# Optimization experiments

Hardware: AMD Instinct MI355X
Metric: run time of the kernel (lower is better)

Reference implementation:

```python
import jax, jax.numpy as jnp
import numpy as np

N, E = 100000, 800000
HID, H, D = 128, 4, 32  # hidden, heads, head_dim (HID = H*D)
NODE_IN, EDGE_IN, NL = 12, 3, 4
EPS_LN = 1e-5


def _ln(x, g, b):
    mu = jnp.mean(x, axis=-1, keepdims=True)
    var = jnp.var(x, axis=-1, keepdims=True)
    return (x - mu) * jax.lax.rsqrt(var + EPS_LN) * g + b


def _gatv2(h, src, dst, e, Wl, bl, Wr, br, We, att, bias):
    # GATv2Conv (PyG semantics): lin_l -> source (x_j), lin_r -> target (x_i)
    xl = (h @ Wl + bl).reshape(-1, H, D)          # (N,H,D) source proj
    xr = (h @ Wr + br).reshape(-1, H, D)          # (N,H,D) target proj
    ee = (e @ We).reshape(-1, H, D)               # (E,H,D) edge proj (no bias in PyG)
    m = xl[src] + xr[dst] + ee                    # (E,H,D)
    score = jnp.einsum('ehd,hd->eh', jax.nn.leaky_relu(m, 0.2), att)  # (E,H)
    smax = jax.ops.segment_max(score, dst, num_segments=N)            # (N,H)
    ex = jnp.exp(score - smax[dst])
    den = jax.ops.segment_sum(ex, dst, num_segments=N)
    alpha = ex / (den[dst] + 1e-16)               # per-destination softmax
    msg = xl[src] * alpha[..., None]              # (E,H,D)
    out = jax.ops.segment_sum(msg, dst, num_segments=N).reshape(-1, H * D)
    return out + bias


def _forward(x, edge_attr, edge_proj_w, edge_proj_b,
             l0_Wl, l0_bl, l0_Wr, l0_br, l0_We, l0_att, l0_bias,
             Wl, bl, Wr, br, We, att, bias, ln_g, ln_b, edge_index):
    src, dst = edge_index[0], edge_index[1]
    e = jax.nn.silu(edge_attr @ edge_proj_w + edge_proj_b)  # (E,HID)
    # layer 0 (12 -> 128): no residual since shapes differ
    hn = _gatv2(x, src, dst, e, l0_Wl, l0_bl, l0_Wr, l0_br, l0_We, l0_att, l0_bias)
    h = jax.nn.silu(_ln(hn, ln_g[0], ln_b[0]))
    for i in range(NL - 1):  # layers 1..3 with residual
        hn = _gatv2(h, src, dst, e, Wl[i], bl[i], Wr[i], br[i], We[i], att[i], bias[i])
        h = h + jax.nn.silu(_ln(hn, ln_g[i + 1], ln_b[i + 1]))
    return h


def setup_inputs():
    key = jax.random.key(0)
    ks = jax.random.split(key, 32)
    g = lambda i, shape, s: (jax.random.normal(ks[i], shape, jnp.float32) * s)
    inp = {
        'x': jax.random.uniform(ks[0], (N, NODE_IN), jnp.float32),
        'edge_index': jax.random.randint(ks[1], (2, E), 0, N, jnp.int32),
        'edge_attr': jax.random.normal(ks[2], (E, EDGE_IN), jnp.float32),
        'edge_proj_w': g(3, (EDGE_IN, HID), 0.3),
        'edge_proj_b': jnp.zeros((HID,), jnp.float32),
        'l0_Wl': g(4, (NODE_IN, HID), 0.2),
        'l0_bl': jnp.zeros((HID,), jnp.float32),
        'l0_Wr': g(5, (NODE_IN, HID), 0.2),
        'l0_br': jnp.zeros((HID,), jnp.float32),
        'l0_We': g(6, (HID, HID), 0.08),
        'l0_att': g(7, (H, D), 0.15),
        'l0_bias': jnp.zeros((HID,), jnp.float32),
        'Wl': g(8, (NL - 1, HID, HID), 0.08),
        'bl': jnp.zeros((NL - 1, HID), jnp.float32),
        'Wr': g(9, (NL - 1, HID, HID), 0.08),
        'br': jnp.zeros((NL - 1, HID), jnp.float32),
        'We': g(10, (NL - 1, HID, HID), 0.08),
        'att': g(11, (NL - 1, H, D), 0.15),
        'bias': jnp.zeros((NL - 1, HID), jnp.float32),
        'ln_g': jnp.ones((NL, HID), jnp.float32),
        'ln_b': jnp.zeros((NL, HID), jnp.float32),
    }
    return inp


def reference(x, edge_index, edge_attr, edge_proj_w, edge_proj_b,
              l0_Wl, l0_bl, l0_Wr, l0_br, l0_We, l0_att, l0_bias,
              Wl, bl, Wr, br, We, att, bias, ln_g, ln_b):
    return _forward(x, edge_attr, edge_proj_w, edge_proj_b,
                    l0_Wl, l0_bl, l0_Wr, l0_br, l0_We, l0_att, l0_bias,
                    Wl, bl, Wr, br, We, att, bias, ln_g, ln_b, edge_index)
```

## Files before the change

### kernel.cpp

```cpp
#include <hip/hip_runtime.h>
#include <hip/hip_bf16.h>


using bf16x8 = __attribute__((ext_vector_type(8))) short;
using f32x4  = __attribute__((ext_vector_type(4))) float;

__device__ inline unsigned short f2bf(float x) {
  __hip_bfloat16 h = __float2bfloat16(x);
  return *reinterpret_cast<unsigned short*>(&h);
}
__device__ inline float bf2f(unsigned short u) {
  unsigned int x = ((unsigned int)u) << 16;
  return __uint_as_float(x);
}

__global__ __launch_bounds__(256) void count_kernel(const int* __restrict__ dstv,
                                                    int* __restrict__ deg, int E) {
  int e = blockIdx.x * 256 + threadIdx.x;
  if (e < E) atomicAdd(&deg[dstv[e]], 1);
}

__global__ __launch_bounds__(1024) void scan_local_kernel(
    const int* __restrict__ deg, int* __restrict__ off,
    int* __restrict__ bsum, int n) {
  __shared__ int wsum[16];
  int t = threadIdx.x;
  int lane = t & 63, wid = t >> 6;
  int i = blockIdx.x * 1024 + t;
  int v = (i < n) ? deg[i] : 0;
  int x = v;
  #pragma unroll
  for (int o = 1; o < 64; o <<= 1) {
    int y = __shfl_up(x, o, 64);
    if (lane >= o) x += y;
  }
  if (lane == 63) wsum[wid] = x;
  __syncthreads();
  if (wid == 0) {
    int w = (lane < 16) ? wsum[lane] : 0;
    #pragma unroll
    for (int o = 1; o < 16; o <<= 1) {
      int y = __shfl_up(w, o, 64);
      if (lane >= o) w += y;
    }
    if (lane < 16) wsum[lane] = w;
  }
  __syncthreads();
  int wbase = (wid == 0) ? 0 : wsum[wid - 1];
  if (i < n) off[i] = wbase + (x - v);
  if (t == 0) bsum[blockIdx.x] = wsum[15];
}

__global__ __launch_bounds__(1024) void scan_bsums_kernel(
    const int* __restrict__ bsum, int* __restrict__ bpre,
    int nb, int* __restrict__ off, int n) {
  __shared__ int wsum[16];
  int t = threadIdx.x;
  int lane = t & 63, wid = t >> 6;
  int v = (t < nb) ? bsum[t] : 0;
  int x = v;
  #pragma unroll
  for (int o = 1; o < 64; o <<= 1) {
    int y = __shfl_up(x, o, 64);
    if (lane >= o) x += y;
  }
  if (lane == 63) wsum[wid] = x;
  __syncthreads();
  if (wid == 0) {
    int w = (lane < 16) ? wsum[lane] : 0;
    #pragma unroll
    for (int o = 1; o < 16; o <<= 1) {
      int y = __shfl_up(w, o, 64);
      if (lane >= o) w += y;
    }
    if (lane < 16) wsum[lane] = w;
  }
  __syncthreads();
  int wbase = (wid == 0) ? 0 : wsum[wid - 1];
  if (t < nb) bpre[t] = wbase + (x - v);
  if (t == 0) off[n] = wsum[15];
}

__global__ __launch_bounds__(256) void scan_addback_kernel(
    int* __restrict__ off, const int* __restrict__ bpre,
    int* __restrict__ cursor, int n) {
  int i = blockIdx.x * 256 + threadIdx.x;
  if (i < n) {
    int v = off[i] + bpre[i >> 10];
    off[i] = v;
    cursor[i] = v;
  }
}

__global__ __launch_bounds__(256) void place_kernel(const int* __restrict__ srcv,
                                                    const int* __restrict__ dstv,
                                                    const float* __restrict__ eattr,
                                                    int* __restrict__ cursor,
                                                    int* __restrict__ ssrc,
                                                    int* __restrict__ sdst,
                                                    float* __restrict__ seattr, int E) {
  int e = blockIdx.x * 256 + threadIdx.x;
  if (e < E) {
    int d = dstv[e];
    int p = atomicAdd(&cursor[d], 1);
    ssrc[p] = srcv[e];
    sdst[p] = d;
    seattr[p * 3 + 0] = eattr[e * 3 + 0];
    seattr[p * 3 + 1] = eattr[e * 3 + 1];
    seattr[p * 3 + 2] = eattr[e * 3 + 2];
  }
}

__global__ __launch_bounds__(256) void wt_kernel(
    const float* __restrict__ l0_We, const float* __restrict__ We,
    const float* __restrict__ Wl, const float* __restrict__ Wr,
    unsigned short* __restrict__ WeT, unsigned short* __restrict__ WlT,
    unsigned short* __restrict__ WrT) {
  int b = blockIdx.x, t = threadIdx.x;
  const float* src;
  unsigned short* dst;
  if (b == 0)      { src = l0_We;              dst = WeT; }
  else if (b < 4)  { src = We + (b - 1) * 16384; dst = WeT + b * 16384; }
  else if (b < 7)  { src = Wl + (b - 4) * 16384; dst = WlT + (b - 4) * 16384; }
  else             { src = Wr + (b - 7) * 16384; dst = WrT + (b - 7) * 16384; }
  int n = t >> 1, k0 = (t & 1) * 64;
  #pragma unroll
  for (int k = 0; k < 64; ++k)
    dst[n * 128 + k0 + k] = f2bf(src[(k0 + k) * 128 + n]);
}

__global__ __launch_bounds__(256) void node_proj0_kernel(
    const float* __restrict__ x,
    const float* __restrict__ Wl, const float* __restrict__ bl,
    const float* __restrict__ Wr, const float* __restrict__ br,
    unsigned short* __restrict__ xl, unsigned short* __restrict__ xr, int N) {
  int idx = blockIdx.x * 256 + threadIdx.x;
  int node = idx >> 7, col = idx & 127;
  if (node >= N) return;
  float al = bl[col], ar = br[col];
  const float* xrow = x + node * 12;
  #pragma unroll
  for (int k = 0; k < 12; ++k) {
    float xv = xrow[k];
    al += xv * Wl[k * 128 + col];
    ar += xv * Wr[k * 128 + col];
  }
  xl[idx] = f2bf(al);
  xr[idx] = f2bf(ar);
}

__global__ __launch_bounds__(256) void node_proj_kernel(
    const unsigned short* __restrict__ hbf,
    const unsigned short* __restrict__ WlT, const float* __restrict__ bl,
    const unsigned short* __restrict__ WrT, const float* __restrict__ br,
    unsigned short* __restrict__ xl, unsigned short* __restrict__ xr, int N) {
  __shared__ unsigned short A_sh[64 * 136];
  int t = threadIdx.x;
  int nb = blockIdx.x * 64;
  #pragma unroll
  for (int it = 0; it < 4; ++it) {
    int idx = it * 256 + t;
    int row = idx >> 4, chunk = idx & 15;
    int ng = nb + row;
    float4 v = make_float4(0.f, 0.f, 0.f, 0.f);
    if (ng < N) v = *(const float4*)(hbf + ng * 128 + chunk * 8);
    *(float4*)(A_sh + row * 136 + chunk * 8) = v;
  }
  __syncthreads();
  int lane = t & 63, w = t >> 6;
  int m = lane & 15, quad = lane >> 4;
  bf16x8 afr[4];
  #pragma unroll
  for (int s = 0; s < 4; ++s)
    afr[s] = *(const bf16x8*)(A_sh + (w * 16 + m) * 136 + s * 32 + quad * 8);
  #pragma unroll
  for (int part = 0; part < 2; ++part) {
    const unsigned short* Bt = part ? WrT : WlT;
    const float* bias = part ? br : bl;
    unsigned short* out = part ? xr : xl;
    f32x4 acc[8];
    #pragma unroll
    for (int tt = 0; tt < 8; ++tt)
      #pragma unroll
      for (int r = 0; r < 4; ++r) acc[tt][r] = 0.f;
    #pragma unroll
    for (int tt = 0; tt < 8; ++tt)
      #pragma unroll
      for (int s = 0; s < 4; ++s) {
        bf16x8 b = *(const bf16x8*)(Bt + (tt * 16 + m) * 128 + s * 32 + quad * 8);
        acc[tt] = __builtin_amdgcn_mfma_f32_16x16x32_bf16(afr[s], b, acc[tt], 0, 0, 0);
      }
    #pragma unroll
    for (int tt = 0; tt < 8; ++tt) {
      int col = tt * 16 + m;
      float bv = bias[col];
      #pragma unroll
      for (int r = 0; r < 4; ++r) {
        int ng = nb + w * 16 + quad * 4 + r;
        if (ng < N) out[ng * 128 + col] = f2bf(acc[tt][r] + bv);
      }
    }
  }
}

__global__ __launch_bounds__(256) void edge_score_kernel(
    const float* __restrict__ seattr,
    const float* __restrict__ Pw,
    const float* __restrict__ Pb,
    const unsigned short* __restrict__ WeT,
    const float* __restrict__ attw,
    const unsigned short* __restrict__ xl, const unsigned short* __restrict__ xr,
    const int* __restrict__ ssrc, const int* __restrict__ sdst,
    float* __restrict__ scores, int E) {
  __shared__ unsigned short ee_sh[64 * 128];
  __shared__ float att_sh[4 * 40];
  __shared__ float pw_sh[512];
  int t = threadIdx.x;
  int eb = blockIdx.x * 64;
  int lane = t & 63, w = t >> 6;
  int m = lane & 15, quad = lane >> 4;

  if (t < 128) att_sh[(t >> 5) * 40 + (t & 31)] = attw[t];
  for (int i = t; i < 512; i += 256) pw_sh[i] = (i < 384) ? Pw[i] : Pb[i - 384];

  int le2 = t >> 2, hh = t & 3;
  int eg = eb + le2;
  int sv = 0, dv = 0;
  if (eg < E) { sv = ssrc[eg]; dv = sdst[eg]; }
  bf16x8 xa[4], xb[4];
  #pragma unroll
  for (int j = 0; j < 4; ++j) {
    xa[j] = *(const bf16x8*)(xl + (size_t)sv * 128 + hh * 32 + j * 8);
    xb[j] = *(const bf16x8*)(xr + (size_t)dv * 128 + hh * 32 + j * 8);
  }
  __builtin_amdgcn_sched_barrier(0);
  __syncthreads();

  int e = eb + w * 16 + m;
  float ea0 = 0.f, ea1 = 0.f, ea2 = 0.f;
  if (e < E) { ea0 = seattr[e * 3]; ea1 = seattr[e * 3 + 1]; ea2 = seattr[e * 3 + 2]; }
  bf16x8 afr[4];
  #pragma unroll
  for (int s = 0; s < 4; ++s) {
    int k0 = s * 32 + quad * 8;
    f32x4 r0a = *(const f32x4*)(pw_sh + k0),       r0b = *(const f32x4*)(pw_sh + k0 + 4);
    f32x4 r1a = *(const f32x4*)(pw_sh + 128 + k0), r1b = *(const f32x4*)(pw_sh + 128 + k0 + 4);
    f32x4 r2a = *(const f32x4*)(pw_sh + 256 + k0), r2b = *(const f32x4*)(pw_sh + 256 + k0 + 4);
    f32x4 r3a = *(const f32x4*)(pw_sh + 384 + k0), r3b = *(const f32x4*)(pw_sh + 384 + k0 + 4);
    union { bf16x8 v; unsigned short u[8]; } af;
    #pragma unroll
    for (int j = 0; j < 4; ++j) {
      float z = ea0 * r0a[j] + ea1 * r1a[j] + ea2 * r2a[j] + r3a[j];
      af.u[j] = f2bf(z * __builtin_amdgcn_rcpf(1.f + __expf(-z)));
      float z2 = ea0 * r0b[j] + ea1 * r1b[j] + ea2 * r2b[j] + r3b[j];
      af.u[j + 4] = f2bf(z2 * __builtin_amdgcn_rcpf(1.f + __expf(-z2)));
    }
    afr[s] = af.v;
  }

  f32x4 acc[8];
  #pragma unroll
  for (int tt = 0; tt < 8; ++tt)
    #pragma unroll
    for (int r = 0; r < 4; ++r) acc[tt][r] = 0.f;
  #pragma unroll
  for (int tt = 0; tt < 8; ++tt)
    #pragma unroll
    for (int s = 0; s < 4; ++s) {
      bf16x8 b = *(const bf16x8*)(WeT + (tt * 16 + m) * 128 + s * 32 + quad * 8);
      acc[tt] = __builtin_amdgcn_mfma_f32_16x16x32_bf16(afr[s], b, acc[tt], 0, 0, 0);
    }

  #pragma unroll
  for (int tt = 0; tt < 8; ++tt) {
    int col = tt * 16 + m;
    int chunk = col >> 3, within = col & 7;
    #pragma unroll
    for (int r = 0; r < 4; ++r) {
      int le = w * 16 + quad * 4 + r;
      int p = chunk ^ (le & 7);
      ee_sh[le * 128 + p * 8 + within] = f2bf(acc[tt][r]);
    }
  }
  __syncthreads();

  if (eg < E) {
    float sc = 0.f;
    #pragma unroll
    for (int cl = 0; cl < 4; ++cl) {
      int p = (hh * 4 + cl) ^ (le2 & 7);
      bf16x8 ev = *(const bf16x8*)(ee_sh + le2 * 128 + p * 8);
      f32x4 av0 = *(const f32x4*)(att_sh + hh * 40 + cl * 8);
      f32x4 av1 = *(const f32x4*)(att_sh + hh * 40 + cl * 8 + 4);
      #pragma unroll
      for (int q = 0; q < 8; ++q) {
        float mv = bf2f((unsigned short)ev[q])
                 + bf2f((unsigned short)xa[cl][q])
                 + bf2f((unsigned short)xb[cl][q]);
        mv = (mv > 0.f) ? mv : 0.2f * mv;
        float aw = (q < 4) ? av0[q] : av1[q - 4];
        sc += mv * aw;
      }
    }
    scores[eg * 4 + hh] = __expf(sc);
  }
}

__global__ __launch_bounds__(256) void aggregate_kernel(
    const unsigned short* __restrict__ xl, const float* __restrict__ scores,
    const int* __restrict__ off, const int* __restrict__ ssrc,
    const float* __restrict__ bias,
    const float* __restrict__ lng, const float* __restrict__ lnb,
    const float* __restrict__ h_in, float* __restrict__ h_out,
    unsigned short* __restrict__ hbf_out, int N) {
  int t = threadIdx.x;
  int wid = t >> 6, lane = t & 63;
  int half = lane >> 5, l32 = lane & 31;
  int n = blockIdx.x * 8 + wid * 2 + half;
  if (n >= N) return;
  int hh = l32 >> 3;
  int col0 = l32 * 4;
  int p0 = off[n], p1 = off[n + 1];
  float den0 = 0.f, den1 = 0.f, den2 = 0.f, den3 = 0.f;
  float a00 = 0.f, a01 = 0.f, a02 = 0.f, a03 = 0.f;
  float a10 = 0.f, a11 = 0.f, a12 = 0.f, a13 = 0.f;
  float a20 = 0.f, a21 = 0.f, a22 = 0.f, a23 = 0.f;
  float a30 = 0.f, a31 = 0.f, a32 = 0.f, a33 = 0.f;
  int p = p0;
  for (; p + 3 < p1; p += 4) {
    float w0 = scores[p * 4 + hh];
    float w1 = scores[(p + 1) * 4 + hh];
    float w2 = scores[(p + 2) * 4 + hh];
    float w3 = scores[(p + 3) * 4 + hh];
    int s0 = ssrc[p], s1 = ssrc[p + 1], s2 = ssrc[p + 2], s3 = ssrc[p + 3];
    ushort4 x0 = *(const ushort4*)(xl + (size_t)s0 * 128 + col0);
    ushort4 x1 = *(const ushort4*)(xl + (size_t)s1 * 128 + col0);
    ushort4 x2 = *(const ushort4*)(xl + (size_t)s2 * 128 + col0);
    ushort4 x3 = *(const ushort4*)(xl + (size_t)s3 * 128 + col0);
    den0 += w0; den1 += w1; den2 += w2; den3 += w3;
    a00 += w0 * bf2f(x0.x); a01 += w0 * bf2f(x0.y); a02 += w0 * bf2f(x0.z); a03 += w0 * bf2f(x0.w);
    a10 += w1 * bf2f(x1.x); a11 += w1 * bf2f(x1.y); a12 += w1 * bf2f(x1.z); a13 += w1 * bf2f(x1.w);
    a20 += w2 * bf2f(x2.x); a21 += w2 * bf2f(x2.y); a22 += w2 * bf2f(x2.z); a23 += w2 * bf2f(x2.w);
    a30 += w3 * bf2f(x3.x); a31 += w3 * bf2f(x3.y); a32 += w3 * bf2f(x3.z); a33 += w3 * bf2f(x3.w);
  }
  for (; p < p1; ++p) {
    float w0 = scores[p * 4 + hh];
    int s0 = ssrc[p];
    ushort4 x0 = *(const ushort4*)(xl + (size_t)s0 * 128 + col0);
    den0 += w0;
    a00 += w0 * bf2f(x0.x); a01 += w0 * bf2f(x0.y); a02 += w0 * bf2f(x0.z); a03 += w0 * bf2f(x0.w);
  }
  float rden = (den0 + den1) + (den2 + den3);
  float c0 = (a00 + a10) + (a20 + a30);
  float c1 = (a01 + a11) + (a21 + a31);
  float c2 = (a02 + a12) + (a22 + a32);
  float c3 = (a03 + a13) + (a23 + a33);
  float inv = 1.f / (rden + 1e-16f);
  const float4 bb = *(const float4*)(bias + col0);
  float v0 = c0 * inv + bb.x;
  float v1 = c1 * inv + bb.y;
  float v2 = c2 * inv + bb.z;
  float v3 = c3 * inv + bb.w;
  float s1 = (v0 + v1) + (v2 + v3);
  float s2 = (v0 * v0 + v1 * v1) + (v2 * v2 + v3 * v3);
  #pragma unroll
  for (int o = 1; o < 32; o <<= 1) {
    s1 += __shfl_xor(s1, o, 64);
    s2 += __shfl_xor(s2, o, 64);
  }
  float mean = s1 * (1.f / 128.f);
  float var = s2 * (1.f / 128.f) - mean * mean;
  float rs = rsqrtf(var + 1e-5f);
  const float4 g4 = *(const float4*)(lng + col0);
  const float4 b4 = *(const float4*)(lnb + col0);
  float y0 = (v0 - mean) * rs * g4.x + b4.x;
  float y1 = (v1 - mean) * rs * g4.y + b4.y;
  float y2 = (v2 - mean) * rs * g4.z + b4.z;
  float y3 = (v3 - mean) * rs * g4.w + b4.w;
  float o0 = y0 / (1.f + __expf(-y0));
  float o1 = y1 / (1.f + __expf(-y1));
  float o2 = y2 / (1.f + __expf(-y2));
  float o3 = y3 / (1.f + __expf(-y3));
  if (h_in) {
    const float4 hv = *(const float4*)(h_in + (size_t)n * 128 + col0);
    o0 += hv.x; o1 += hv.y; o2 += hv.z; o3 += hv.w;
  }
  float4 ov; ov.x = o0; ov.y = o1; ov.z = o2; ov.w = o3;
  *(float4*)(h_out + (size_t)n * 128 + col0) = ov;
  if (hbf_out) {
    ushort4 hb;
    hb.x = f2bf(o0); hb.y = f2bf(o1); hb.z = f2bf(o2); hb.w = f2bf(o3);
    *(ushort4*)(hbf_out + (size_t)n * 128 + col0) = hb;
  }
}

extern "C" void kernel_launch(void* const* d_in, const int* in_sizes, int n_in,
                              void* d_out, int out_size, void* d_ws, size_t ws_size,
                              hipStream_t stream) {
  const float* x       = (const float*)d_in[0];
  const int*   eidx    = (const int*)d_in[1];
  const float* eattr   = (const float*)d_in[2];
  const float* Pw      = (const float*)d_in[3];
  const float* Pb      = (const float*)d_in[4];
  const float* l0_Wl   = (const float*)d_in[5];
  const float* l0_bl   = (const float*)d_in[6];
  const float* l0_Wr   = (const float*)d_in[7];
  const float* l0_br   = (const float*)d_in[8];
  const float* l0_We   = (const float*)d_in[9];
  const float* l0_att  = (const float*)d_in[10];
  const float* l0_bias = (const float*)d_in[11];
  const float* Wl      = (const float*)d_in[12];
  const float* bl      = (const float*)d_in[13];
  const float* Wr      = (const float*)d_in[14];
  const float* br      = (const float*)d_in[15];
  const float* We      = (const float*)d_in[16];
  const float* att     = (const float*)d_in[17];
  const float* bias    = (const float*)d_in[18];
  const float* ln_g    = (const float*)d_in[19];
  const float* ln_b    = (const float*)d_in[20];
  (void)n_in; (void)out_size; (void)ws_size;

  int N = in_sizes[0] / 12;
  int E = in_sizes[2] / 3;
  const int* srcv = eidx;
  const int* dstv = eidx + E;

  char* w = (char*)d_ws;
  unsigned short* xl_bf = (unsigned short*)w; w += (size_t)N * 128 * 2;
  unsigned short* xr_bf = (unsigned short*)w; w += (size_t)N * 128 * 2;
  unsigned short* h_bf  = (unsigned short*)w; w += (size_t)N * 128 * 2;
  float* h      = (float*)w;  w += (size_t)N * 128 * 4;
  float* scores = (float*)w;  w += (size_t)E * 4 * 4;
  float* seattr = (float*)w;  w += (size_t)E * 3 * 4;
  int* ssrc   = (int*)w;      w += (size_t)E * 4;
  int* sdst   = (int*)w;      w += (size_t)E * 4;
  int* deg    = (int*)w;      w += (size_t)N * 4;
  int* off    = (int*)w;      w += (size_t)(N + 1) * 4;
  int* cursor = (int*)w;      w += (size_t)N * 4 + 12;
  unsigned short* WeT = (unsigned short*)w; w += (size_t)4 * 16384 * 2;
  unsigned short* WlT = (unsigned short*)w; w += (size_t)3 * 16384 * 2;
  unsigned short* WrT = (unsigned short*)w; w += (size_t)3 * 16384 * 2;

  int* bsum = (int*)scores;
  int* bpre = (int*)scores + 1024;

  hipMemsetAsync(deg, 0, (size_t)N * 4, stream);
  int gE = (E + 255) / 256;
  count_kernel<<<gE, 256, 0, stream>>>(dstv, deg, E);
  int nb = (N + 1023) / 1024;
  scan_local_kernel<<<nb, 1024, 0, stream>>>(deg, off, bsum, N);
  scan_bsums_kernel<<<1, 1024, 0, stream>>>(bsum, bpre, nb, off, N);
  scan_addback_kernel<<<(N + 255) / 256, 256, 0, stream>>>(off, bpre, cursor, N);
  place_kernel<<<gE, 256, 0, stream>>>(srcv, dstv, eattr, cursor, ssrc, sdst, seattr, E);
  wt_kernel<<<10, 256, 0, stream>>>(l0_We, We, Wl, Wr, WeT, WlT, WrT);

  dim3 egrid((E + 63) / 64);
  dim3 ngrid((N + 63) / 64);
  int agrid = (N + 7) / 8;

  node_proj0_kernel<<<(N * 128 + 255) / 256, 256, 0, stream>>>(
      x, l0_Wl, l0_bl, l0_Wr, l0_br, xl_bf, xr_bf, N);
  edge_score_kernel<<<egrid, 256, 0, stream>>>(
      seattr, Pw, Pb, WeT, l0_att, xl_bf, xr_bf, ssrc, sdst, scores, E);
  aggregate_kernel<<<agrid, 256, 0, stream>>>(
      xl_bf, scores, off, ssrc, l0_bias, ln_g, ln_b, nullptr, h, h_bf, N);

  for (int i = 0; i < 3; ++i) {
    node_proj_kernel<<<ngrid, 256, 0, stream>>>(
        h_bf, WlT + i * 16384, bl + i * 128, WrT + i * 16384, br + i * 128,
        xl_bf, xr_bf, N);
    edge_score_kernel<<<egrid, 256, 0, stream>>>(
        seattr, Pw, Pb, WeT + (i + 1) * 16384, att + i * 128,
        xl_bf, xr_bf, ssrc, sdst, scores, E);
    float* hout = (i == 2) ? (float*)d_out : h;
    unsigned short* hbfout = (i == 2) ? nullptr : h_bf;
    aggregate_kernel<<<agrid, 256, 0, stream>>>(
        xl_bf, scores, off, ssrc, bias + i * 128,
        ln_g + (i + 1) * 128, ln_b + (i + 1) * 128, h, hout, hbfout, N);
  }
}
```

Measured before the change: 1.515 ms.

## Process two edge tiles per block in edge_score, prefetching second tile's gathers

The edge score kernel now handles 128 edges per block in two 64-edge halves. The xl/xr gathers and edge attributes for the second half are issued before scoring the first half, so their latency overlaps with compute. The shared-memory setup (att, projection weights) is also amortized over twice as many edges. In exchange, register pressure rises from holding two sets of gathered rows, the grid has half as many blocks, and an extra barrier is added.

```diff
diff --git a/kernel.cpp b/kernel.cpp
--- a/kernel.cpp
+++ b/kernel.cpp
@@ -216,7 +216,7 @@
   __shared__ float att_sh[4 * 40];
   __shared__ float pw_sh[512];
   int t = threadIdx.x;
-  int eb = blockIdx.x * 64;
+  int eb = blockIdx.x * 128;
   int lane = t & 63, w = t >> 6;
   int m = lane & 15, quad = lane >> 4;
 
@@ -224,21 +224,22 @@
   for (int i = t; i < 512; i += 256) pw_sh[i] = (i < 384) ? Pw[i] : Pb[i - 384];
 
   int le2 = t >> 2, hh = t & 3;
-  int eg = eb + le2;
-  int sv = 0, dv = 0;
-  if (eg < E) { sv = ssrc[eg]; dv = sdst[eg]; }
-  bf16x8 xa[4], xb[4];
+
+  int egA = eb + le2;
+  int svA = 0, dvA = 0;
+  if (egA < E) { svA = ssrc[egA]; dvA = sdst[egA]; }
+  bf16x8 xaA[4], xbA[4];
   #pragma unroll
   for (int j = 0; j < 4; ++j) {
-    xa[j] = *(const bf16x8*)(xl + (size_t)sv * 128 + hh * 32 + j * 8);
-    xb[j] = *(const bf16x8*)(xr + (size_t)dv * 128 + hh * 32 + j * 8);
+    xaA[j] = *(const bf16x8*)(xl + (size_t)svA * 128 + hh * 32 + j * 8);
+    xbA[j] = *(const bf16x8*)(xr + (size_t)dvA * 128 + hh * 32 + j * 8);
   }
   __builtin_amdgcn_sched_barrier(0);
   __syncthreads();
 
-  int e = eb + w * 16 + m;
-  float ea0 = 0.f, ea1 = 0.f, ea2 = 0.f;
-  if (e < E) { ea0 = seattr[e * 3]; ea1 = seattr[e * 3 + 1]; ea2 = seattr[e * 3 + 2]; }
+  int eA = eb + w * 16 + m;
+  float a0 = 0.f, a1 = 0.f, a2 = 0.f;
+  if (eA < E) { a0 = seattr[eA * 3]; a1 = seattr[eA * 3 + 1]; a2 = seattr[eA * 3 + 2]; }
   bf16x8 afr[4];
   #pragma unroll
   for (int s = 0; s < 4; ++s) {
@@ -250,14 +251,13 @@
     union { bf16x8 v; unsigned short u[8]; } af;
     #pragma unroll
     for (int j = 0; j < 4; ++j) {
-      float z = ea0 * r0a[j] + ea1 * r1a[j] + ea2 * r2a[j] + r3a[j];
+      float z = a0 * r0a[j] + a1 * r1a[j] + a2 * r2a[j] + r3a[j];
       af.u[j] = f2bf(z * __builtin_amdgcn_rcpf(1.f + __expf(-z)));
-      float z2 = ea0 * r0b[j] + ea1 * r1b[j] + ea2 * r2b[j] + r3b[j];
+      float z2 = a0 * r0b[j] + a1 * r1b[j] + a2 * r2b[j] + r3b[j];
       af.u[j + 4] = f2bf(z2 * __builtin_amdgcn_rcpf(1.f + __expf(-z2)));
     }
     afr[s] = af.v;
   }
-
   f32x4 acc[8];
   #pragma unroll
   for (int tt = 0; tt < 8; ++tt)
@@ -270,7 +270,6 @@
       bf16x8 b = *(const bf16x8*)(WeT + (tt * 16 + m) * 128 + s * 32 + quad * 8);
       acc[tt] = __builtin_amdgcn_mfma_f32_16x16x32_bf16(afr[s], b, acc[tt], 0, 0, 0);
     }
-
   #pragma unroll
   for (int tt = 0; tt < 8; ++tt) {
     int col = tt * 16 + m;
@@ -284,7 +283,21 @@
   }
   __syncthreads();
 
-  if (eg < E) {
+  int egB = eb + 64 + le2;
+  int svB = 0, dvB = 0;
+  if (egB < E) { svB = ssrc[egB]; dvB = sdst[egB]; }
+  bf16x8 xaB[4], xbB[4];
+  #pragma unroll
+  for (int j = 0; j < 4; ++j) {
+    xaB[j] = *(const bf16x8*)(xl + (size_t)svB * 128 + hh * 32 + j * 8);
+    xbB[j] = *(const bf16x8*)(xr + (size_t)dvB * 128 + hh * 32 + j * 8);
+  }
+  int eB = eb + 64 + w * 16 + m;
+  float b0 = 0.f, b1 = 0.f, b2 = 0.f;
+  if (eB < E) { b0 = seattr[eB * 3]; b1 = seattr[eB * 3 + 1]; b2 = seattr[eB * 3 + 2]; }
+  __builtin_amdgcn_sched_barrier(0);
+
+  if (egA < E) {
     float sc = 0.f;
     #pragma unroll
     for (int cl = 0; cl < 4; ++cl) {
@@ -295,14 +308,77 @@
       #pragma unroll
       for (int q = 0; q < 8; ++q) {
         float mv = bf2f((unsigned short)ev[q])
-                 + bf2f((unsigned short)xa[cl][q])
-                 + bf2f((unsigned short)xb[cl][q]);
+                 + bf2f((unsigned short)xaA[cl][q])
+                 + bf2f((unsigned short)xbA[cl][q]);
         mv = (mv > 0.f) ? mv : 0.2f * mv;
         float aw = (q < 4) ? av0[q] : av1[q - 4];
         sc += mv * aw;
       }
     }
-    scores[eg * 4 + hh] = __expf(sc);
+    scores[egA * 4 + hh] = __expf(sc);
+  }
+
+  #pragma unroll
+  for (int s = 0; s < 4; ++s) {
+    int k0 = s * 32 + quad * 8;
+    f32x4 r0a = *(const f32x4*)(pw_sh + k0),       r0b = *(const f32x4*)(pw_sh + k0 + 4);
+    f32x4 r1a = *(const f32x4*)(pw_sh + 128 + k0), r1b = *(const f32x4*)(pw_sh + 128 + k0 + 4);
+    f32x4 r2a = *(const f32x4*)(pw_sh + 256 + k0), r2b = *(const f32x4*)(pw_sh + 256 + k0 + 4);
+    f32x4 r3a = *(const f32x4*)(pw_sh + 384 + k0), r3b = *(const f32x4*)(pw_sh + 384 + k0 + 4);
+    union { bf16x8 v; unsigned short u[8]; } af;
+    #pragma unroll
+    for (int j = 0; j < 4; ++j) {
+      float z = b0 * r0a[j] + b1 * r1a[j] + b2 * r2a[j] + r3a[j];
+      af.u[j] = f2bf(z * __builtin_amdgcn_rcpf(1.f + __expf(-z)));
+      float z2 = b0 * r0b[j] + b1 * r1b[j] + b2 * r2b[j] + r3b[j];
+      af.u[j + 4] = f2bf(z2 * __builtin_amdgcn_rcpf(1.f + __expf(-z2)));
+    }
+    afr[s] = af.v;
+  }
+  #pragma unroll
+  for (int tt = 0; tt < 8; ++tt)
+    #pragma unroll
+    for (int r = 0; r < 4; ++r) acc[tt][r] = 0.f;
+  #pragma unroll
+  for (int tt = 0; tt < 8; ++tt)
+    #pragma unroll
+    for (int s = 0; s < 4; ++s) {
+      bf16x8 b = *(const bf16x8*)(WeT + (tt * 16 + m) * 128 + s * 32 + quad * 8);
+      acc[tt] = __builtin_amdgcn_mfma_f32_16x16x32_bf16(afr[s], b, acc[tt], 0, 0, 0);
+    }
+  __syncthreads();
+  #pragma unroll
+  for (int tt = 0; tt < 8; ++tt) {
+    int col = tt * 16 + m;
+    int chunk = col >> 3, within = col & 7;
+    #pragma unroll
+    for (int r = 0; r < 4; ++r) {
+      int le = w * 16 + quad * 4 + r;
+      int p = chunk ^ (le & 7);
+      ee_sh[le * 128 + p * 8 + within] = f2bf(acc[tt][r]);
+    }
+  }
+  __syncthreads();
+
+  if (egB < E) {
+    float sc = 0.f;
+    #pragma unroll
+    for (int cl = 0; cl < 4; ++cl) {
+      int p = (hh * 4 + cl) ^ (le2 & 7);
+      bf16x8 ev = *(const bf16x8*)(ee_sh + le2 * 128 + p * 8);
+      f32x4 av0 = *(const f32x4*)(att_sh + hh * 40 + cl * 8);
+      f32x4 av1 = *(const f32x4*)(att_sh + hh * 40 + cl * 8 + 4);
+      #pragma unroll
+      for (int q = 0; q < 8; ++q) {
+        float mv = bf2f((unsigned short)ev[q])
+                 + bf2f((unsigned short)xaB[cl][q])
+                 + bf2f((unsigned short)xbB[cl][q]);
+        mv = (mv > 0.f) ? mv : 0.2f * mv;
+        float aw = (q < 4) ? av0[q] : av1[q - 4];
+        sc += mv * aw;
+      }
+    }
+    scores[egB * 4 + hh] = __expf(sc);
   }
 }
 
@@ -454,7 +530,7 @@
   place_kernel<<<gE, 256, 0, stream>>>(srcv, dstv, eattr, cursor, ssrc, sdst, seattr, E);
   wt_kernel<<<10, 256, 0, stream>>>(l0_We, We, Wl, Wr, WeT, WlT, WrT);
 
-  dim3 egrid((E + 63) / 64);
+  dim3 egrid((E + 127) / 128);
   dim3 ngrid((N + 63) / 64);
   int agrid = (N + 7) / 8;
 
```

Measured after the change: 1.660 ms. 1.1x slower.
